# Optimization experiments

Measured on AMD Instinct MI355X. Metric: run time of the kernel, lower is better.

The kernel has to match this reference:

```python
import jax, jax.numpy as jnp
from jax import lax
import numpy as np

C = 64          # in_channels == out_channels (residual add requires it)
K = 3           # kernel_size
DIL = 2         # dilation
PAD = (K + (DIL - 1) * (K - 1)) // 2  # reflection padding = 2
MORPH = 2 * DIL + 1                    # morphology kernel size = 5


def _reflect_pad(x):
    return jnp.pad(x, ((0, 0), (0, 0), (PAD, PAD), (PAD, PAD)), mode='reflect')


def _conv(x, w, groups=1):
    # NCHW / OIHW, stride 1, VALID padding (padding already applied), dilated kernel
    return lax.conv_general_dilated(
        x, w, window_strides=(1, 1), padding='VALID',
        rhs_dilation=(DIL, DIL),
        dimension_numbers=('NCHW', 'OIHW', 'NCHW'),
        feature_group_count=groups)


def _binary_dilate(m):
    # kornia.morphology.dilation with an all-ones (2*dil+1)^2 structuring element
    # on a {0,1} mask == max-pool with SAME padding.
    return lax.reduce_window(m, -jnp.inf, lax.max,
                             (1, 1, MORPH, MORPH), (1, 1, 1, 1), 'SAME')


def setup_inputs() -> dict:
    key = jax.random.key(0)
    k1, k2, k3, k4, k5, k6, k7, k8 = jax.random.split(key, 8)
    B, H, W = 1, 512, 512
    x = jax.random.normal(k1, (B, C, H, W), dtype=jnp.float32)
    mask = (jax.random.uniform(k2, (B, 1, H, W)) > 0.5).astype(jnp.float32)
    fan = 1.0 / np.sqrt(C * K * K)
    w1 = jax.random.uniform(k3, (C, C, K, K), minval=-fan, maxval=fan, dtype=jnp.float32)
    b1 = jax.random.uniform(k4, (C,), minval=-fan, maxval=fan, dtype=jnp.float32)
    w2 = jax.random.uniform(k5, (C, C, K, K), minval=-fan, maxval=fan, dtype=jnp.float32)
    b2 = jax.random.uniform(k6, (C,), minval=-fan, maxval=fan, dtype=jnp.float32)
    fan_dw = 1.0 / np.sqrt(K * K)  # depthwise: c_in per group = 1
    w3 = jax.random.uniform(k7, (C, 1, K, K), minval=-fan_dw, maxval=fan_dw, dtype=jnp.float32)
    b3 = jax.random.uniform(k8, (C,), minval=-fan_dw, maxval=fan_dw, dtype=jnp.float32)
    return {'x': x, 'mask': mask, 'w1': w1, 'b1': b1, 'w2': w2, 'b2': b2, 'w3': w3, 'b3': b3}


def reference(x, mask, w1, b1, w2, b2, w3, b3):
    # Eval-mode DynConvLayer forward. The original gathers unfold patches at
    # mask-selected pixels, applies the conv via einsum, and scatters back;
    # mathematically this equals a full conv followed by a masked select, which
    # is the faithful dense equivalent implemented here.
    gelu = lambda t: jax.nn.gelu(t, approximate=False)  # torch nn.GELU (exact)

    md = _binary_dilate(mask) > 0.5  # dilated-mask positions (B,1,H,W)
    sd = mask > 0.5                  # shadow positions

    # conv2d at md positions, scattered into x -> x_ori
    out1 = gelu(_conv(_reflect_pad(x), w1) + b1[None, :, None, None])
    x_ori = jnp.where(md, out1, x)

    # augment_conv2d on the updated tensor, taken at sd positions
    out2 = gelu(_conv(_reflect_pad(x_ori), w2) + b2[None, :, None, None])

    # depthwise light_conv2d on the ORIGINAL x, taken at ~sd positions
    out3 = gelu(_conv(_reflect_pad(x), w3, groups=C) + b3[None, :, None, None])

    # x_ori[sd] = out2; x_ori[~sd] = out3  (sd and ~sd partition all pixels)
    x_ori = jnp.where(sd, out2, out3)
    return x_ori + x
```

## Files before the change

### kernel.cpp

```cpp
#include <hip/hip_runtime.h>

#define Hdim 512
#define Wdim 512
#define Cdim 64
#define HWSZ (Hdim * Wdim)
#define TH 8
#define TW 32
#define IH 12
#define IW 36
#define NL (IH * IW)

typedef __attribute__((ext_vector_type(8))) short short8;
typedef __attribute__((ext_vector_type(4))) float f32x4;
typedef __attribute__((ext_vector_type(4))) int   i32x4;

__device__ __forceinline__ int reflect_idx(int i) {
    i = abs(i);
    if (i >= Hdim) i = 2 * Hdim - 2 - i;
    return i;
}

__device__ __forceinline__ unsigned bf16_1(float f) {
    unsigned u = __float_as_uint(f);
    return (u + 0x7FFF + ((u >> 16) & 1)) >> 16;
}
__device__ __forceinline__ unsigned bf16pk(float lo, float hi) {
    return bf16_1(lo) | (bf16_1(hi) << 16);
}
__device__ __forceinline__ float gelu_fast(float v) {
    float u = v * fmaf(v * v, 0.0713548162726f, 1.59576912161f);
    float e = __expf(-u);
    return v / (1.0f + e);
}

template <int MODE>
__global__ __launch_bounds__(256, 2) void mconv(
    const float* __restrict__ xin_f,
    const unsigned short* __restrict__ xin_t,
    const float* __restrict__ mask,
    const float* __restrict__ wgt,
    const float* __restrict__ bias,
    const float* __restrict__ xres,
    unsigned short* __restrict__ out_t,
    float* __restrict__ out_f)
{
    __shared__ unsigned char sx[NL * 80];
    __shared__ unsigned char wlds[5 * 4 * 1024];
    __shared__ float smask[NL];

    const int tid  = threadIdx.x;
    const int lane = tid & 63;
    const int wv   = tid >> 6;
    const int bx   = blockIdx.x & 15;
    const int by   = blockIdx.x >> 4;
    const int ox0  = bx * TW, oy0 = by * TH;

    f32x4 acc[4][4];
    #pragma unroll
    for (int fr = 0; fr < 4; ++fr) {
        f32x4 b;
        #pragma unroll
        for (int r = 0; r < 4; ++r) b[r] = bias[fr * 16 + (lane >> 4) * 4 + r];
        #pragma unroll
        for (int fc = 0; fc < 4; ++fc) acc[fr][fc] = b;
    }

    if (MODE == 0) {
        for (int i = tid; i < NL; i += 256) {
            int r = oy0 - 2 + i / IW, c = ox0 - 2 + (i - (i / IW) * IW);
            float m = 0.0f;
            if (r >= 0 && r < Hdim && c >= 0 && c < Wdim) m = mask[r * Wdim + c];
            smask[i] = m;
        }
    }

    auto stage_input = [&](int h) __attribute__((always_inline)) {
        if (MODE == 0) {
            int s  = (lane >> 3) & 3;
            int Lo = (lane & 7) + ((lane >> 5) << 3);
            #pragma unroll
            for (int it = 0; it < 7; ++it) {
                int L = it * 64 + wv * 16 + Lo;
                if (L < NL) {
                    int r  = reflect_idx(oy0 - 2 + L / IW);
                    int c  = reflect_idx(ox0 - 2 + (L - (L / IW) * IW));
                    int gp = r * Wdim + c;
                    #pragma unroll
                    for (int jk = 0; jk < 4; ++jk) {
                        int ci = h * 32 + jk * 8 + s * 2;
                        float f0 = xin_f[ci * HWSZ + gp];
                        float f1 = xin_f[(ci + 1) * HWSZ + gp];
                        *(unsigned*)&sx[L * 80 + jk * 16 + s * 4] = bf16pk(f0, f1);
                    }
                }
            }
        } else {
            #pragma unroll
            for (int it = 0; it < 7; ++it) {
                int L  = it * 64 + wv * 16 + (lane >> 2);
                int jk = lane & 3;
                if (L < NL) {
                    int r  = reflect_idx(oy0 - 2 + L / IW);
                    int c  = reflect_idx(ox0 - 2 + (L - (L / IW) * IW));
                    int gp = r * Wdim + c;
                    i32x4 v = *(const i32x4*)&xin_t[gp * 64 + h * 32 + jk * 8];
                    *(i32x4*)&sx[L * 80 + jk * 16] = v;
                }
            }
        }
    };

    auto stage_w = [&](int h, int t0, int nt) __attribute__((always_inline)) {
        for (int q = tid; q < nt * 256; q += 256) {
            int f = q >> 6, l = q & 63;
            int tt = f >> 2, fr = f & 3;
            int co = fr * 16 + (l & 15);
            int ci = h * 32 + ((l >> 4) << 3);
            const float* wp = wgt + (co * 64 + ci) * 9 + (t0 + tt);
            i32x4 v;
            v.x = bf16pk(wp[0],  wp[9]);
            v.y = bf16pk(wp[18], wp[27]);
            v.z = bf16pk(wp[36], wp[45]);
            v.w = bf16pk(wp[54], wp[63]);
            *(i32x4*)&wlds[q * 16] = v;
        }
    };

    auto compute = [&](int t0, int nt) __attribute__((always_inline)) {
        #pragma unroll
        for (int tt = 0; tt < nt; ++tt) {
            int t = t0 + tt;
            int dy = (t / 3) * 2, dx = (t - (t / 3) * 3) * 2;
            short8 af[4], bfr[4];
            #pragma unroll
            for (int fr = 0; fr < 4; ++fr)
                af[fr] = *(const short8*)&wlds[(tt * 4 + fr) * 1024 + lane * 16];
            #pragma unroll
            for (int fc = 0; fc < 4; ++fc) {
                int pr = 2 * wv + (fc >> 1);
                int pc = (fc & 1) * 16 + (lane & 15);
                int L  = (pr + dy) * IW + pc + dx;
                bfr[fc] = *(const short8*)&sx[L * 80 + (lane >> 4) * 16];
            }
            #pragma unroll
            for (int fr = 0; fr < 4; ++fr)
                #pragma unroll
                for (int fc = 0; fc < 4; ++fc)
                    acc[fr][fc] = __builtin_amdgcn_mfma_f32_16x16x32_bf16(
                        af[fr], bfr[fc], acc[fr][fc], 0, 0, 0);
        }
    };

    stage_input(0); stage_w(0, 0, 5);
    __syncthreads();
    compute(0, 5);
    __syncthreads();
    stage_w(0, 5, 4);
    __syncthreads();
    compute(5, 4);
    __syncthreads();
    stage_input(1); stage_w(1, 0, 5);
    __syncthreads();
    compute(0, 5);
    __syncthreads();
    stage_w(1, 5, 4);
    __syncthreads();
    compute(5, 4);

    if (MODE == 0) {
        float mdv;
        {
            int pr = 2 * wv + (lane >> 5), pc = lane & 31;
            float m = 0.0f;
            #pragma unroll
            for (int dy = 0; dy < 5; ++dy)
                #pragma unroll
                for (int dx = 0; dx < 5; ++dx)
                    m = fmaxf(m, smask[(pr + dy) * IW + pc + dx]);
            mdv = m;
        }
        __syncthreads();
        unsigned char* bounce = sx + wv * 8192;
        #pragma unroll
        for (int fc = 0; fc < 4; ++fc) {
            float msel = __shfl(mdv, fc * 16 + (lane & 15), 64);
            bool md = msel > 0.5f;
            int p = fc * 16 + (lane & 15);
            int gpix = (oy0 + 2 * wv + (p >> 5)) * Wdim + ox0 + (p & 31);
            int g = lane >> 4;
            #pragma unroll
            for (int fr = 0; fr < 4; ++fr) {
                int co0 = fr * 16 + g * 4;
                unsigned pk0, pk1;
                if (md) {
                    pk0 = bf16pk(gelu_fast(acc[fr][fc][0]), gelu_fast(acc[fr][fc][1]));
                    pk1 = bf16pk(gelu_fast(acc[fr][fc][2]), gelu_fast(acc[fr][fc][3]));
                } else {
                    pk0 = bf16pk(xres[(co0 + 0) * HWSZ + gpix], xres[(co0 + 1) * HWSZ + gpix]);
                    pk1 = bf16pk(xres[(co0 + 2) * HWSZ + gpix], xres[(co0 + 3) * HWSZ + gpix]);
                }
                int cj = fr * 2 + (g >> 1);
                int bo = p * 128 + ((cj ^ (p & 7)) * 16) + (g & 1) * 8;
                *(unsigned*)&bounce[bo]     = pk0;
                *(unsigned*)&bounce[bo + 4] = pk1;
            }
        }
        __syncthreads();
        #pragma unroll
        for (int q = 0; q < 8; ++q) {
            int m   = (q & 3) * 64 + lane;
            int row = 2 * wv + (q >> 2);
            int pp  = (q >> 2) * 32 + (m >> 3);
            int j   = m & 7;
            i32x4 v = *(const i32x4*)&bounce[pp * 128 + ((j ^ (pp & 7)) * 16)];
            *(i32x4*)&out_t[((size_t)((oy0 + row) * Wdim + ox0)) * 64 + m * 8] = v;
        }
    } else {
        #pragma unroll
        for (int fc = 0; fc < 4; ++fc) {
            int p = fc * 16 + (lane & 15);
            int gpix = (oy0 + 2 * wv + (p >> 5)) * Wdim + ox0 + (p & 31);
            bool sd = mask[gpix] > 0.5f;
            if (sd) {
                #pragma unroll
                for (int fr = 0; fr < 4; ++fr) {
                    int co0 = fr * 16 + (lane >> 4) * 4;
                    #pragma unroll
                    for (int r = 0; r < 4; ++r) {
                        float v = gelu_fast(acc[fr][fc][r]) + xres[(co0 + r) * HWSZ + gpix];
                        out_f[(co0 + r) * HWSZ + gpix] = v;
                    }
                }
            }
        }
    }
}

__global__ __launch_bounds__(256) void dwk(
    const float* __restrict__ x, const float* __restrict__ mask,
    const float* __restrict__ w3, const float* __restrict__ b3,
    float* __restrict__ out)
{
    int pix = blockIdx.x * 256 + threadIdx.x;
    int r = pix >> 9, c = pix & 511;
    if (mask[pix] > 0.5f) return;
    int ro[3] = { reflect_idx(r - 2) * Wdim, r * Wdim, reflect_idx(r + 2) * Wdim };
    int co[3] = { reflect_idx(c - 2), c, reflect_idx(c + 2) };
    for (int ci = 0; ci < Cdim; ++ci) {
        const float* xp = x + ci * HWSZ;
        const float* wp = w3 + ci * 9;
        float s = b3[ci];
        float xc = 0.0f;
        #pragma unroll
        for (int a = 0; a < 3; ++a)
            #pragma unroll
            for (int b = 0; b < 3; ++b) {
                float xv = xp[ro[a] + co[b]];
                if (a == 1 && b == 1) xc = xv;
                s = fmaf(xv, wp[a * 3 + b], s);
            }
        out[ci * HWSZ + pix] = gelu_fast(s) + xc;
    }
}

extern "C" void kernel_launch(void* const* d_in, const int* in_sizes, int n_in,
                              void* d_out, int out_size, void* d_ws, size_t ws_size,
                              hipStream_t stream) {
    const float* x    = (const float*)d_in[0];
    const float* mask = (const float*)d_in[1];
    const float* w1   = (const float*)d_in[2];
    const float* b1   = (const float*)d_in[3];
    const float* w2   = (const float*)d_in[4];
    const float* b2   = (const float*)d_in[5];
    const float* w3   = (const float*)d_in[6];
    const float* b3   = (const float*)d_in[7];
    float* out = (float*)d_out;
    unsigned short* xori = (unsigned short*)d_ws;

    const int nblk = (Hdim / TH) * (Wdim / TW);

    mconv<0><<<nblk, 256, 0, stream>>>(x, nullptr, mask, w1, b1, x, xori, nullptr);
    mconv<1><<<nblk, 256, 0, stream>>>(nullptr, xori, mask, w2, b2, x, nullptr, out);
    dwk<<<HWSZ / 256, 256, 0, stream>>>(x, mask, w3, b3, out);
}
```

Baseline: 354.9 us.

## Pre-transpose input to bf16 NHWC and stage all channels with async LDS loads

Adds a transpose kernel that converts x into a channel-last bf16 buffer, which both conv passes and the depthwise kernel then read. The conv kernel now stages the full 64-channel halo tile once through global_load_lds with an XOR swizzle, and double-buffers per-tap weights inside a 9-iteration loop instead of two half-channel passes with many barriers. The depthwise kernel reads vectorized bf16 channel chunks and writes through an LDS transpose for coalesced stores. The aim is to remove strided fp32 gathers and redundant staging. In exchange it adds an extra pass over x, larger LDS use, and bf16 precision on the depthwise path.

Result: slower. 371.2 us (+4.6%).

```diff
diff --git a/kernel.cpp b/kernel.cpp
--- a/kernel.cpp
+++ b/kernel.cpp
@@ -9,6 +9,11 @@
 #define IH 12
 #define IW 36
 #define NL (IH * IW)
+#define NCHUNK (NL * 8)
+#define SX_BYTES (NL * 128)
+#define WB_OFF SX_BYTES
+#define SMASK_OFF (SX_BYTES + 16384)
+#define LDS_TOTAL (SMASK_OFF + NL * 4)
 
 typedef __attribute__((ext_vector_type(8))) short short8;
 typedef __attribute__((ext_vector_type(4))) float f32x4;
@@ -19,7 +24,6 @@
     if (i >= Hdim) i = 2 * Hdim - 2 - i;
     return i;
 }
-
 __device__ __forceinline__ unsigned bf16_1(float f) {
     unsigned u = __float_as_uint(f);
     return (u + 0x7FFF + ((u >> 16) & 1)) >> 16;
@@ -29,13 +33,34 @@
 }
 __device__ __forceinline__ float gelu_fast(float v) {
     float u = v * fmaf(v * v, 0.0713548162726f, 1.59576912161f);
-    float e = __expf(-u);
-    return v / (1.0f + e);
+    return v / (1.0f + __expf(-u));
+}
+__device__ __forceinline__ void gl16(const void* g, void* l) {
+    __builtin_amdgcn_global_load_lds(
+        (const __attribute__((address_space(1))) unsigned int*)g,
+        (__attribute__((address_space(3))) unsigned int*)l, 16, 0, 0);
+}
+
+__global__ __launch_bounds__(256) void tposek(
+    const float* __restrict__ x, unsigned short* __restrict__ xbf)
+{
+    const int lane = threadIdx.x & 63, wv = threadIdx.x >> 6;
+    const int pix = blockIdx.x * 256 + wv * 64 + lane;
+    #pragma unroll
+    for (int q = 0; q < 8; ++q) {
+        unsigned pk[4];
+        #pragma unroll
+        for (int k = 0; k < 4; ++k) {
+            float f0 = x[(q * 8 + 2 * k    ) * HWSZ + pix];
+            float f1 = x[(q * 8 + 2 * k + 1) * HWSZ + pix];
+            pk[k] = bf16pk(f0, f1);
+        }
+        *(i32x4*)&xbf[(size_t)pix * 64 + q * 8] = *(const i32x4*)pk;
+    }
 }
 
 template <int MODE>
 __global__ __launch_bounds__(256, 2) void mconv(
-    const float* __restrict__ xin_f,
     const unsigned short* __restrict__ xin_t,
     const float* __restrict__ mask,
     const float* __restrict__ wgt,
@@ -44,9 +69,8 @@
     unsigned short* __restrict__ out_t,
     float* __restrict__ out_f)
 {
-    __shared__ unsigned char sx[NL * 80];
-    __shared__ unsigned char wlds[5 * 4 * 1024];
-    __shared__ float smask[NL];
+    __shared__ __align__(16) unsigned char lds[LDS_TOTAL];
+    float* smask = (float*)(lds + SMASK_OFF);
 
     const int tid  = threadIdx.x;
     const int lane = tid & 63;
@@ -65,6 +89,37 @@
         for (int fc = 0; fc < 4; ++fc) acc[fr][fc] = b;
     }
 
+    #pragma unroll 1
+    for (int it = 0; it < 14; ++it) {
+        int qb = it * 256 + wv * 64;
+        if (qb < NCHUNK) {
+            int q = qb + lane;
+            int L = q >> 3, j = q & 7;
+            int tr = L / IW, tc = L - tr * IW;
+            int r = reflect_idx(oy0 - 2 + tr);
+            int c = reflect_idx(ox0 - 2 + tc);
+            int jj = j ^ (L & 7);
+            gl16(xin_t + ((size_t)(r * Wdim + c) << 6) + (jj << 3),
+                 (void*)(lds + qb * 16 + lane * 16));
+        }
+    }
+    {
+        unsigned char* wb = lds + WB_OFF;
+        #pragma unroll
+        for (int it = 0; it < 2; ++it) {
+            int q = it * 256 + tid;
+            int h = q >> 8, f = (q >> 6) & 3, l = q & 63;
+            int co = f * 16 + (l & 15);
+            int ci = h * 32 + ((l >> 4) << 3);
+            const float* wp = wgt + (co * 64 + ci) * 9 + 0;
+            i32x4 v;
+            v.x = bf16pk(wp[0],  wp[9]);
+            v.y = bf16pk(wp[18], wp[27]);
+            v.z = bf16pk(wp[36], wp[45]);
+            v.w = bf16pk(wp[54], wp[63]);
+            *(i32x4*)&wb[q * 16] = v;
+        }
+    }
     if (MODE == 0) {
         for (int i = tid; i < NL; i += 256) {
             int r = oy0 - 2 + i / IW, c = ox0 - 2 + (i - (i / IW) * IW);
@@ -73,99 +128,55 @@
             smask[i] = m;
         }
     }
-
-    auto stage_input = [&](int h) __attribute__((always_inline)) {
-        if (MODE == 0) {
-            int s  = (lane >> 3) & 3;
-            int Lo = (lane & 7) + ((lane >> 5) << 3);
-            #pragma unroll
-            for (int it = 0; it < 7; ++it) {
-                int L = it * 64 + wv * 16 + Lo;
-                if (L < NL) {
-                    int r  = reflect_idx(oy0 - 2 + L / IW);
-                    int c  = reflect_idx(ox0 - 2 + (L - (L / IW) * IW));
-                    int gp = r * Wdim + c;
+    __syncthreads();
+
+    #pragma unroll 1
+    for (int t = 0; t < 9; ++t) {
+        if (t < 8) {
+            const int tn = t + 1;
+            unsigned char* wb = lds + WB_OFF + (tn & 1) * 8192;
+            #pragma unroll
+            for (int it = 0; it < 2; ++it) {
+                int q = it * 256 + tid;
+                int h = q >> 8, f = (q >> 6) & 3, l = q & 63;
+                int co = f * 16 + (l & 15);
+                int ci = h * 32 + ((l >> 4) << 3);
+                const float* wp = wgt + (co * 64 + ci) * 9 + tn;
+                i32x4 v;
+                v.x = bf16pk(wp[0],  wp[9]);
+                v.y = bf16pk(wp[18], wp[27]);
+                v.z = bf16pk(wp[36], wp[45]);
+                v.w = bf16pk(wp[54], wp[63]);
+                *(i32x4*)&wb[q * 16] = v;
+            }
+        }
+        {
+            const unsigned char* wb = lds + WB_OFF + (t & 1) * 8192;
+            const int dy = (t / 3) * 2, dx = (t % 3) * 2;
+            #pragma unroll
+            for (int h = 0; h < 2; ++h) {
+                short8 af[4], bfr[4];
+                #pragma unroll
+                for (int fr = 0; fr < 4; ++fr)
+                    af[fr] = *(const short8*)&wb[h * 4096 + fr * 1024 + lane * 16];
+                #pragma unroll
+                for (int fc = 0; fc < 4; ++fc) {
+                    int prr = 2 * wv + (fc >> 1) + dy;
+                    int pcc = (fc & 1) * 16 + (lane & 15) + dx;
+                    int L = prr * IW + pcc;
+                    int cpos = (h * 4 + (lane >> 4)) ^ (L & 7);
+                    bfr[fc] = *(const short8*)&lds[L * 128 + cpos * 16];
+                }
+                #pragma unroll
+                for (int fr = 0; fr < 4; ++fr)
                     #pragma unroll
-                    for (int jk = 0; jk < 4; ++jk) {
-                        int ci = h * 32 + jk * 8 + s * 2;
-                        float f0 = xin_f[ci * HWSZ + gp];
-                        float f1 = xin_f[(ci + 1) * HWSZ + gp];
-                        *(unsigned*)&sx[L * 80 + jk * 16 + s * 4] = bf16pk(f0, f1);
-                    }
-                }
-            }
-        } else {
-            #pragma unroll
-            for (int it = 0; it < 7; ++it) {
-                int L  = it * 64 + wv * 16 + (lane >> 2);
-                int jk = lane & 3;
-                if (L < NL) {
-                    int r  = reflect_idx(oy0 - 2 + L / IW);
-                    int c  = reflect_idx(ox0 - 2 + (L - (L / IW) * IW));
-                    int gp = r * Wdim + c;
-                    i32x4 v = *(const i32x4*)&xin_t[gp * 64 + h * 32 + jk * 8];
-                    *(i32x4*)&sx[L * 80 + jk * 16] = v;
-                }
-            }
-        }
-    };
-
-    auto stage_w = [&](int h, int t0, int nt) __attribute__((always_inline)) {
-        for (int q = tid; q < nt * 256; q += 256) {
-            int f = q >> 6, l = q & 63;
-            int tt = f >> 2, fr = f & 3;
-            int co = fr * 16 + (l & 15);
-            int ci = h * 32 + ((l >> 4) << 3);
-            const float* wp = wgt + (co * 64 + ci) * 9 + (t0 + tt);
-            i32x4 v;
-            v.x = bf16pk(wp[0],  wp[9]);
-            v.y = bf16pk(wp[18], wp[27]);
-            v.z = bf16pk(wp[36], wp[45]);
-            v.w = bf16pk(wp[54], wp[63]);
-            *(i32x4*)&wlds[q * 16] = v;
-        }
-    };
-
-    auto compute = [&](int t0, int nt) __attribute__((always_inline)) {
-        #pragma unroll
-        for (int tt = 0; tt < nt; ++tt) {
-            int t = t0 + tt;
-            int dy = (t / 3) * 2, dx = (t - (t / 3) * 3) * 2;
-            short8 af[4], bfr[4];
-            #pragma unroll
-            for (int fr = 0; fr < 4; ++fr)
-                af[fr] = *(const short8*)&wlds[(tt * 4 + fr) * 1024 + lane * 16];
-            #pragma unroll
-            for (int fc = 0; fc < 4; ++fc) {
-                int pr = 2 * wv + (fc >> 1);
-                int pc = (fc & 1) * 16 + (lane & 15);
-                int L  = (pr + dy) * IW + pc + dx;
-                bfr[fc] = *(const short8*)&sx[L * 80 + (lane >> 4) * 16];
-            }
-            #pragma unroll
-            for (int fr = 0; fr < 4; ++fr)
-                #pragma unroll
-                for (int fc = 0; fc < 4; ++fc)
-                    acc[fr][fc] = __builtin_amdgcn_mfma_f32_16x16x32_bf16(
-                        af[fr], bfr[fc], acc[fr][fc], 0, 0, 0);
-        }
-    };
-
-    stage_input(0); stage_w(0, 0, 5);
-    __syncthreads();
-    compute(0, 5);
-    __syncthreads();
-    stage_w(0, 5, 4);
-    __syncthreads();
-    compute(5, 4);
-    __syncthreads();
-    stage_input(1); stage_w(1, 0, 5);
-    __syncthreads();
-    compute(0, 5);
-    __syncthreads();
-    stage_w(1, 5, 4);
-    __syncthreads();
-    compute(5, 4);
+                    for (int fc = 0; fc < 4; ++fc)
+                        acc[fr][fc] = __builtin_amdgcn_mfma_f32_16x16x32_bf16(
+                            af[fr], bfr[fc], acc[fr][fc], 0, 0, 0);
+            }
+        }
+        __syncthreads();
+    }
 
     if (MODE == 0) {
         float mdv;
@@ -180,7 +191,7 @@
             mdv = m;
         }
         __syncthreads();
-        unsigned char* bounce = sx + wv * 8192;
+        unsigned char* bounce = lds + wv * 8192;
         #pragma unroll
         for (int fc = 0; fc < 4; ++fc) {
             float msel = __shfl(mdv, fc * 16 + (lane & 15), 64);
@@ -237,29 +248,60 @@
 }
 
 __global__ __launch_bounds__(256) void dwk(
-    const float* __restrict__ x, const float* __restrict__ mask,
+    const unsigned short* __restrict__ xbf,
+    const float* __restrict__ mask,
     const float* __restrict__ w3, const float* __restrict__ b3,
     float* __restrict__ out)
 {
-    int pix = blockIdx.x * 256 + threadIdx.x;
-    int r = pix >> 9, c = pix & 511;
-    if (mask[pix] > 0.5f) return;
-    int ro[3] = { reflect_idx(r - 2) * Wdim, r * Wdim, reflect_idx(r + 2) * Wdim };
-    int co[3] = { reflect_idx(c - 2), c, reflect_idx(c + 2) };
-    for (int ci = 0; ci < Cdim; ++ci) {
-        const float* xp = x + ci * HWSZ;
-        const float* wp = w3 + ci * 9;
-        float s = b3[ci];
-        float xc = 0.0f;
-        #pragma unroll
-        for (int a = 0; a < 3; ++a)
+    __shared__ __align__(16) unsigned char sb[32 * 256];
+    const int tid = threadIdx.x;
+    const int pl = tid >> 3, j = tid & 7;
+    const int pix0 = blockIdx.x * 32;
+    const int gpix = pix0 + pl;
+    const int r = gpix >> 9, c = gpix & 511;
+    const int ci0 = j * 8;
+
+    if (mask[gpix] <= 0.5f) {
+        float s[8], resid[8];
+        #pragma unroll
+        for (int k = 0; k < 8; ++k) s[k] = b3[ci0 + k];
+        #pragma unroll
+        for (int a = 0; a < 3; ++a) {
+            int rr = reflect_idx(r - 2 + 2 * a);
             #pragma unroll
             for (int b = 0; b < 3; ++b) {
-                float xv = xp[ro[a] + co[b]];
-                if (a == 1 && b == 1) xc = xv;
-                s = fmaf(xv, wp[a * 3 + b], s);
-            }
-        out[ci * HWSZ + pix] = gelu_fast(s) + xc;
+                int cc = reflect_idx(c - 2 + 2 * b);
+                i32x4 v = *(const i32x4*)&xbf[(size_t)(rr * Wdim + cc) * 64 + ci0];
+                const unsigned* u = (const unsigned*)&v;
+                #pragma unroll
+                for (int k = 0; k < 4; ++k) {
+                    float f0 = __uint_as_float(u[k] << 16);
+                    float f1 = __uint_as_float(u[k] & 0xFFFF0000u);
+                    s[2 * k]     = fmaf(f0, w3[(ci0 + 2 * k) * 9 + a * 3 + b], s[2 * k]);
+                    s[2 * k + 1] = fmaf(f1, w3[(ci0 + 2 * k + 1) * 9 + a * 3 + b], s[2 * k + 1]);
+                    if (a == 1 && b == 1) { resid[2 * k] = f0; resid[2 * k + 1] = f1; }
+                }
+            }
+        }
+        #pragma unroll
+        for (int half = 0; half < 2; ++half) {
+            f32x4 o;
+            #pragma unroll
+            for (int k = 0; k < 4; ++k) o[k] = gelu_fast(s[half * 4 + k]) + resid[half * 4 + k];
+            int q0 = j * 2 + half;
+            *(f32x4*)&sb[pl * 256 + ((q0 ^ (pl & 15)) * 16)] = o;
+        }
+    }
+    __syncthreads();
+    #pragma unroll
+    for (int it = 0; it < 8; ++it) {
+        int m = it * 256 + tid;
+        int co = m >> 5, p = m & 31;
+        if (mask[pix0 + p] <= 0.5f) {
+            int qq = co >> 2;
+            float v = *(const float*)&sb[p * 256 + ((qq ^ (p & 15)) * 16) + (co & 3) * 4];
+            out[co * HWSZ + pix0 + p] = v;
+        }
     }
 }
 
@@ -275,11 +317,14 @@
     const float* w3   = (const float*)d_in[6];
     const float* b3   = (const float*)d_in[7];
     float* out = (float*)d_out;
-    unsigned short* xori = (unsigned short*)d_ws;
+
+    unsigned short* xbf  = (unsigned short*)d_ws;
+    unsigned short* xori = (unsigned short*)((char*)d_ws + 33554432);
 
     const int nblk = (Hdim / TH) * (Wdim / TW);
 
-    mconv<0><<<nblk, 256, 0, stream>>>(x, nullptr, mask, w1, b1, x, xori, nullptr);
-    mconv<1><<<nblk, 256, 0, stream>>>(nullptr, xori, mask, w2, b2, x, nullptr, out);
-    dwk<<<HWSZ / 256, 256, 0, stream>>>(x, mask, w3, b3, out);
-}
+    tposek<<<HWSZ / 256, 256, 0, stream>>>(x, xbf);
+    mconv<0><<<nblk, 256, 0, stream>>>(xbf,  mask, w1, b1, x, xori, nullptr);
+    mconv<1><<<nblk, 256, 0, stream>>>(xori, mask, w2, b2, x, nullptr, out);
+    dwk<<<HWSZ / 32, 256, 0, stream>>>(xbf, mask, w3, b3, out);
+}
```
